# Kernel tuning notes

Measured on AMD Instinct MI355X. Metric: run time of the kernel, lower is better.

Reference implementation:

```python
import jax, jax.numpy as jnp
import numpy as np

SLOPE = 0.2  # leaky_relu_slope for both LVC block and kernel predictor (passed through)
DILATIONS = (1, 3, 9, 27)
HOP = 256
STRIDE = 8
IN_CH = 32
KSZ = 3  # conv_kernel_size


def conv1d(x, w, b, dilation=1, padding=0):
    # x: (B,C,T), w: (O,I,K) torch layout
    y = jax.lax.conv_general_dilated(
        x, w, window_strides=(1,), padding=[(padding, padding)],
        rhs_dilation=(dilation,), dimension_numbers=('NCH', 'OIH', 'NCH'))
    return y + b[None, :, None]


def conv_transpose1d(x, w, b, stride, padding, output_padding=0):
    # w: torch ConvTranspose1d layout (Cin, Cout, K)
    w_ = jnp.flip(w, -1).transpose(1, 0, 2)  # (Cout, Cin, K)
    K = w.shape[2]
    pad = (K - 1 - padding, K - 1 - padding + output_padding)
    y = jax.lax.conv_general_dilated(
        x, w_, window_strides=(1,), padding=[pad],
        lhs_dilation=(stride,), dimension_numbers=('NCH', 'OIH', 'NCH'))
    return y + b[None, :, None]


def lrelu(x, slope=SLOPE):
    return jnp.where(x >= 0, x, slope * x)


def location_variable_convolution(x, kernel, bias, hop):
    # x: (B,C,T), kernel: (B,C,O,k,L), bias: (B,O,L); T == L*hop; dilation==1 path
    B, C, T = x.shape
    _, _, O, k, L = kernel.shape
    pad = (k - 1) // 2
    xp = jnp.pad(x, ((0, 0), (0, 0), (pad, pad)))
    # gather per-segment sliding windows: (L, hop, k) index into time axis
    idx = (jnp.arange(L)[:, None, None] * hop
           + jnp.arange(hop)[None, :, None]
           + jnp.arange(k)[None, None, :])
    xw = xp[:, :, idx]  # (B, C, L, hop, k)
    o = jnp.einsum('bclsk,bcokl->bols', xw, kernel)  # (B, O, L, hop)
    o = o + bias[:, :, :, None]
    return o.reshape(B, O, L * hop)


def kernel_predictor(spec, kp_in_w, kp_in_b, rb_w1, rb_b1, rb_w2, rb_b2,
                     kern_w, kern_b, bias_w, bias_b):
    B, _, L = spec.shape
    h = conv1d(spec, kp_in_w, kp_in_b, padding=2)  # k=5, pad=2
    for i in range(3):  # num_blocks = 3
        r = h
        h = conv1d(h, rb_w1[i], rb_b1[i], padding=1)
        h = lrelu(h)
        h = conv1d(h, rb_w2[i], rb_b2[i], padding=1)
        h = lrelu(h) + r
    kh = conv1d(h, kern_w, kern_b, padding=1)
    bh = conv1d(h, bias_w, bias_b, padding=1)
    n_layers = len(DILATIONS)
    kernels = kh.reshape(B, n_layers, IN_CH, 2 * IN_CH, KSZ, L)
    biases = bh.reshape(B, n_layers, 2 * IN_CH, L)
    return kernels, biases


def reference(hidden_states, spectrogram, convt_w, convt_b, kp_in_w, kp_in_b,
              rb_w1, rb_b1, rb_w2, rb_b2, kern_w, kern_b, bias_w, bias_b,
              lvc_w, lvc_b):
    h = conv_transpose1d(hidden_states, convt_w, convt_b,
                         stride=STRIDE, padding=STRIDE // 2 + STRIDE % 2,
                         output_padding=STRIDE % 2)
    kernels, biases = kernel_predictor(spectrogram, kp_in_w, kp_in_b,
                                       rb_w1, rb_b1, rb_w2, rb_b2,
                                       kern_w, kern_b, bias_w, bias_b)
    for i, d in enumerate(DILATIONS):
        r = h
        h = lrelu(h)
        h = conv1d(h, lvc_w[i], lvc_b[i], dilation=d, padding=d * (KSZ - 1) // 2)
        h = lrelu(h)
        h = location_variable_convolution(h, kernels[:, i], biases[:, i], HOP)
        h = jax.nn.sigmoid(h[:, :IN_CH, :]) * jnp.tanh(h[:, IN_CH:, :]) + r
    return h


def setup_inputs() -> dict:
    key = jax.random.key(0)
    ks = jax.random.split(key, 12)
    B, COND, L, H = 4, 100, 256, 64
    T = L * HOP  # 65536 output samples
    s = jnp.float32(0.02)
    d = {}
    d['hidden_states'] = jax.random.normal(ks[0], (B, IN_CH, T // STRIDE), jnp.float32)
    d['spectrogram'] = jax.random.normal(ks[1], (B, COND, L), jnp.float32)
    d['convt_w'] = jax.random.normal(ks[2], (IN_CH, IN_CH, 2 * STRIDE), jnp.float32) * s
    d['convt_b'] = jnp.zeros((IN_CH,), jnp.float32)
    d['kp_in_w'] = jax.random.normal(ks[3], (H, COND, 5), jnp.float32) * s
    d['kp_in_b'] = jnp.zeros((H,), jnp.float32)
    d['rb_w1'] = jax.random.normal(ks[4], (3, H, H, 3), jnp.float32) * s
    d['rb_b1'] = jnp.zeros((3, H), jnp.float32)
    d['rb_w2'] = jax.random.normal(ks[5], (3, H, H, 3), jnp.float32) * s
    d['rb_b2'] = jnp.zeros((3, H), jnp.float32)
    KC = IN_CH * 2 * IN_CH * KSZ * len(DILATIONS)  # 24576
    d['kern_w'] = jax.random.normal(ks[6], (KC, H, 3), jnp.float32) * s
    d['kern_b'] = jnp.zeros((KC,), jnp.float32)
    BC = 2 * IN_CH * len(DILATIONS)  # 256
    d['bias_w'] = jax.random.normal(ks[7], (BC, H, 3), jnp.float32) * s
    d['bias_b'] = jnp.zeros((BC,), jnp.float32)
    d['lvc_w'] = jax.random.normal(ks[8], (len(DILATIONS), IN_CH, IN_CH, 3), jnp.float32) * s
    d['lvc_b'] = jnp.zeros((len(DILATIONS), IN_CH), jnp.float32)
    return d
```

## Files before the change

### kernel.cpp

```cpp
#include <hip/hip_runtime.h>
#include <math.h>

#define NB 4
#define T 65536
#define TIN 8192
#define LL 256
#define KCL 6144

__device__ __forceinline__ float lrelu_f(float v) { return v >= 0.f ? v : 0.2f * v; }

union Phase1LDS {
    struct { float xs[32][264]; float wm[64][128]; } cvt;
    struct { float hs[64][56]; float xsp[20][56]; float wt[192][68]; } trk;
};

__global__ void __launch_bounds__(512) phase1(
    const float* __restrict__ x, const float* __restrict__ cw,
    const float* __restrict__ cbias, float* __restrict__ hout,
    const float* __restrict__ spec,
    const float* __restrict__ kp_in_w, const float* __restrict__ kp_in_b,
    const float* __restrict__ rb_w1, const float* __restrict__ rb_b1,
    const float* __restrict__ rb_w2, const float* __restrict__ rb_b2,
    float* __restrict__ kp_h) {
    __shared__ Phase1LDS u;
    const int bid = blockIdx.x;
    const int tid = threadIdx.x;
    const int lane = tid & 63, wv = tid >> 6;

    if (bid < 264) {
        const int bx = bid % 33;
        const int rr = bid / 33;
        const int mtp = rr & 1;
        const int b = rr >> 1;
        const int s0base = bx * 256;
        float (*xs)[264] = u.cvt.xs;
        float (*wm)[128] = u.cvt.wm;

        const float* xb = x + (size_t)b * 32 * TIN;
        for (int idx = tid; idx < 32 * 64; idx += 512) {
            int c = idx >> 6, q = idx & 63;
            int p = s0base + q * 4;
            float4 v = (p + 3 < TIN) ? *(const float4*)(xb + c * TIN + p)
                                     : make_float4(0.f, 0.f, 0.f, 0.f);
            *(float4*)&xs[c][4 + 4 * q] = v;
        }
        if (tid < 32) {
            int p = s0base - 1;
            xs[tid][3] = (p >= 0) ? xb[tid * TIN + p] : 0.f;
        }
        for (int idx = tid; idx < 8192; idx += 512) {
            int i = idx >> 7, mm = idx & 127;
            int oo = mtp * 16 + (mm >> 3), k0 = mm & 7;
            wm[i][mm] = (i < 32) ? cw[i * 512 + oo * 16 + k0]
                                 : cw[(i - 32) * 512 + oo * 16 + k0 + 8];
        }
        __syncthreads();

        float acc[2][8][4];
#pragma unroll
        for (int ol = 0; ol < 2; ++ol) {
            float bo = cbias[mtp * 16 + wv * 2 + ol];
#pragma unroll
            for (int k0 = 0; k0 < 8; ++k0)
#pragma unroll
                for (int si = 0; si < 4; ++si) acc[ol][k0][si] = bo;
        }

        for (int c = 0; c < 32; ++c) {
            float xm1[4], x0[4];
#pragma unroll
            for (int si = 0; si < 4; ++si) {
                xm1[si] = xs[c][lane + si * 64 + 3];
                x0[si]  = xs[c][lane + si * 64 + 4];
            }
            float w0[16], w1[16];
#pragma unroll
            for (int q = 0; q < 4; ++q) {
                *(float4*)&w0[q * 4] = *(const float4*)&wm[c][wv * 16 + q * 4];
                *(float4*)&w1[q * 4] = *(const float4*)&wm[32 + c][wv * 16 + q * 4];
            }
#pragma unroll
            for (int ol = 0; ol < 2; ++ol)
#pragma unroll
                for (int k0 = 0; k0 < 8; ++k0)
#pragma unroll
                    for (int si = 0; si < 4; ++si)
                        acc[ol][k0][si] += x0[si] * w0[ol * 8 + k0] + xm1[si] * w1[ol * 8 + k0];
        }

#pragma unroll
        for (int ol = 0; ol < 2; ++ol) {
            float* ob = hout + ((size_t)b * 32 + mtp * 16 + wv * 2 + ol) * T;
#pragma unroll
            for (int si = 0; si < 4; ++si) {
                int tb = (s0base + lane + si * 64) * 8 - 4;
                if (tb >= 0 && tb < T)
                    *(float4*)(ob + tb) = make_float4(acc[ol][0][si], acc[ol][1][si],
                                                      acc[ol][2][si], acc[ol][3][si]);
                if (tb + 4 >= 0 && tb + 4 < T)
                    *(float4*)(ob + tb + 4) = make_float4(acc[ol][4][si], acc[ol][5][si],
                                                          acc[ol][6][si], acc[ol][7][si]);
            }
        }
        return;
    }

    const int tb = bid - 264;
    const int lq = tb & 7, b = tb >> 3;
    const int j = lane;
    const int oc0 = wv * 8;
    const int l0 = lq * 32;
    const int labs = l0 - 9 + j;
    const bool lvalid = (labs >= 0 && labs < 256);

    float (*hs)[56] = u.trk.hs;
    float (*xsp)[56] = u.trk.xsp;
    float (*wt)[68] = u.trk.wt;

    float pw[24];
    float px[3];

    auto pf_kpin = [&](int cc) {
#pragma unroll
        for (int t = 0; t < 13; ++t) {
            int idx = t * 512 + tid;
            pw[t] = 0.f;
            if (idx < 6400) pw[t] = kp_in_w[(size_t)(idx / 100) * 500 + cc * 100 + (idx % 100)];
        }
    };
    auto wr_kpin = [&]() {
#pragma unroll
        for (int t = 0; t < 13; ++t) {
            int idx = t * 512 + tid;
            if (idx < 6400) wt[idx % 100][idx / 100] = pw[t];
        }
    };
    auto pf_xsp = [&](int cc) {
#pragma unroll
        for (int t = 0; t < 3; ++t) {
            int idx = t * 512 + tid;
            px[t] = 0.f;
            if (idx < 1120) {
                int c = idx / 56, jj = idx - c * 56;
                int l = l0 - 9 + jj;
                if (l >= 0 && l < 256)
                    px[t] = spec[((size_t)b * 100 + cc * 20 + c) * LL + l];
            }
        }
    };
    auto wr_xsp = [&]() {
#pragma unroll
        for (int t = 0; t < 3; ++t) {
            int idx = t * 512 + tid;
            if (idx < 1120) xsp[idx / 56][idx % 56] = px[t];
        }
    };
    auto pf_w192 = [&](const float* src) {
#pragma unroll
        for (int t = 0; t < 24; ++t) pw[t] = src[t * 512 + tid];
    };
    auto wr_w192 = [&]() {
#pragma unroll
        for (int t = 0; t < 24; ++t) {
            int idx = t * 512 + tid;
            wt[idx % 192][idx / 192] = pw[t];
        }
    };
    auto conv64 = [&](int jlo, int jhi, const float* bptr, float* a) {
#pragma unroll
        for (int oi = 0; oi < 8; ++oi) a[oi] = bptr[oc0 + oi];
        if (j >= jlo && j < jhi) {
            for (int c = 0; c < 64; ++c) {
                float x0 = hs[c][j - 1], x1 = hs[c][j], x2 = hs[c][j + 1];
#pragma unroll
                for (int k = 0; k < 3; ++k) {
                    float xk = (k == 0) ? x0 : (k == 1) ? x1 : x2;
                    float w8[8];
                    *(float4*)&w8[0] = *(const float4*)&wt[c * 3 + k][oc0];
                    *(float4*)&w8[4] = *(const float4*)&wt[c * 3 + k][oc0 + 4];
#pragma unroll
                    for (int oi = 0; oi < 8; ++oi) a[oi] += xk * w8[oi];
                }
            }
        }
    };

    pf_kpin(0); pf_xsp(0);
    wr_kpin(); wr_xsp();
    __syncthreads();

    float acc[8];
#pragma unroll
    for (int oi = 0; oi < 8; ++oi) acc[oi] = kp_in_b[oc0 + oi];

    for (int cc = 0; cc < 5; ++cc) {
        if (cc < 4) { pf_kpin(cc + 1); pf_xsp(cc + 1); }
        else        { pf_w192(rb_w1); }
        if (j >= 2 && j < 48) {
            for (int c = 0; c < 20; ++c) {
                float x5[5];
#pragma unroll
                for (int u2 = 0; u2 < 5; ++u2) x5[u2] = xsp[c][j - 2 + u2];
#pragma unroll
                for (int k = 0; k < 5; ++k) {
                    float w8[8];
                    *(float4*)&w8[0] = *(const float4*)&wt[c * 5 + k][oc0];
                    *(float4*)&w8[4] = *(const float4*)&wt[c * 5 + k][oc0 + 4];
#pragma unroll
                    for (int oi = 0; oi < 8; ++oi) acc[oi] += x5[k] * w8[oi];
                }
            }
        }
        if (cc == 4 && j >= 2 && j < 48) {
#pragma unroll
            for (int oi = 0; oi < 8; ++oi) hs[oc0 + oi][j] = lvalid ? acc[oi] : 0.f;
        }
        __syncthreads();
        if (cc < 4) { wr_kpin(); wr_xsp(); }
        else        { wr_w192(); }
        __syncthreads();
    }

    for (int i = 0; i < 3; ++i) {
        const int jlo1 = 3 + 2 * i, jhi1 = 47 - 2 * i;
        const int jlo2 = jlo1 + 1, jhi2 = jhi1 - 1;
        float r[8];
        if (j >= jlo2 && j < jhi2) {
#pragma unroll
            for (int oi = 0; oi < 8; ++oi) r[oi] = hs[oc0 + oi][j];
        }
        pf_w192(rb_w2 + (size_t)i * 12288);
        float a1[8];
        conv64(jlo1, jhi1, rb_b1 + i * 64, a1);
        __syncthreads();
        if (j >= jlo1 && j < jhi1) {
#pragma unroll
            for (int oi = 0; oi < 8; ++oi) hs[oc0 + oi][j] = lvalid ? lrelu_f(a1[oi]) : 0.f;
        }
        wr_w192();
        __syncthreads();
        if (i < 2) pf_w192(rb_w1 + (size_t)(i + 1) * 12288);
        float a2[8];
        conv64(jlo2, jhi2, rb_b2 + i * 64, a2);
        __syncthreads();
        if (j >= jlo2 && j < jhi2) {
#pragma unroll
            for (int oi = 0; oi < 8; ++oi) hs[oc0 + oi][j] = lvalid ? (lrelu_f(a2[oi]) + r[oi]) : 0.f;
        }
        if (i < 2) wr_w192();
        __syncthreads();
    }

    for (int idx = tid; idx < 64 * 32; idx += 512) {
        int c = idx >> 5, jj = idx & 31;
        kp_h[((size_t)b * 64 + c) * LL + l0 + jj] = hs[c][9 + jj];
    }
}

__device__ __forceinline__ void khead_core(
    int bx, int b, int tid,
    const float* __restrict__ kp_h, const float* __restrict__ kw,
    const float* __restrict__ kb, const float* __restrict__ bias_w,
    const float* __restrict__ bias_b, float* __restrict__ kh,
    float* __restrict__ bh, int layer,
    float (*xs)[264], float (*ws)[36]) {
    const bool isbias = (bx >= 192);
    const int lane = tid & 63, wv = tid >> 6;
    int g = 0, oc0 = 0, ci = 0, kk = 0, ocb0 = 0;
    const float* wsrc;
    size_t wrow0;
    int wstride;
    if (!isbias) {
        g = bx >> 1; oc0 = (bx & 1) * 32;
        ci = g / 3; kk = g - ci * 3;
        wsrc = kw + (size_t)layer * KCL * 192;
        wrow0 = (size_t)((ci * 64 + oc0) * 3 + kk) * 192;
        wstride = 576;
    } else {
        ocb0 = (bx - 192) * 32;
        wsrc = bias_w;
        wrow0 = (size_t)ocb0 * 192;
        wstride = 192;
    }
    const int oc4w = wv * 4;

    float acc[4][4];
#pragma unroll
    for (int oi = 0; oi < 4; ++oi) {
        float bv = isbias ? bias_b[ocb0 + oc4w + oi]
                          : kb[layer * KCL + (ci * 64 + oc0 + oc4w + oi) * 3 + kk];
#pragma unroll
        for (int q = 0; q < 4; ++q) acc[oi][q] = bv;
    }

    for (int half = 0; half < 2; ++half) {
        const int hc0 = half * 32;
        __syncthreads();
        for (int idx = tid; idx < 32 * 64; idx += 512) {
            int c = idx >> 6, q = idx & 63;
            *(float4*)&xs[c][4 + 4 * q] =
                *(const float4*)(kp_h + ((size_t)b * 64 + hc0 + c) * LL + 4 * q);
        }
        if (tid < 32) { xs[tid][3] = 0.f; xs[tid][260] = 0.f; }
        for (int idx = tid; idx < 3072; idx += 512) {
            int ocl = idx / 96, jj = idx - ocl * 96;
            ws[jj][ocl] = wsrc[wrow0 + (size_t)ocl * wstride + hc0 * 3 + jj];
        }
        __syncthreads();
        for (int c = 0; c < 32; ++c) {
            float4 xa = *(const float4*)&xs[c][4 * lane];
            float4 xm = *(const float4*)&xs[c][4 + 4 * lane];
            float4 xb = *(const float4*)&xs[c][8 + 4 * lane];
            float xx[6] = {xa.w, xm.x, xm.y, xm.z, xm.w, xb.x};
#pragma unroll
            for (int t = 0; t < 3; ++t) {
                float4 w4 = *(const float4*)&ws[c * 3 + t][oc4w];
#pragma unroll
                for (int q = 0; q < 4; ++q) {
                    acc[0][q] += w4.x * xx[q + t];
                    acc[1][q] += w4.y * xx[q + t];
                    acc[2][q] += w4.z * xx[q + t];
                    acc[3][q] += w4.w * xx[q + t];
                }
            }
        }
    }

    if (!isbias) {
#pragma unroll
        for (int q = 0; q < 4; ++q) {
            int l = 4 * lane + q;
            float* op = kh + ((size_t)b * LL + l) * KCL + g * 64 + oc0 + oc4w;
            *(float4*)op = make_float4(acc[0][q], acc[1][q], acc[2][q], acc[3][q]);
        }
    } else {
#pragma unroll
        for (int oi = 0; oi < 4; ++oi) {
            float* op = bh + ((size_t)b * 256 + ocb0 + oc4w + oi) * LL + 4 * lane;
            *(float4*)op = make_float4(acc[oi][0], acc[oi][1], acc[oi][2], acc[oi][3]);
        }
    }
}

__global__ void __launch_bounds__(512, 2) kern_head512(
    const float* __restrict__ kp_h, const float* __restrict__ kw,
    const float* __restrict__ kb, const float* __restrict__ bias_w,
    const float* __restrict__ bias_b, float* __restrict__ kh,
    float* __restrict__ bh, int layer) {
    __shared__ float xs[32][264];
    __shared__ float ws[96][36];
    khead_core(blockIdx.x, blockIdx.y, threadIdx.x, kp_h, kw, kb, bias_w, bias_b,
               kh, bh, layer, xs, ws);
}

__device__ __forceinline__ void lf_core(
    int l, int b, int tid,
    const float* __restrict__ kh, const float* __restrict__ bh,
    const float* __restrict__ w, const float* __restrict__ bias,
    const float* __restrict__ hin, float* __restrict__ hout,
    int layer, int dil,
    float (*xh)[316], float* ks, float (*ws)[36]) {
    const int lane = tid & 63, wv = tid >> 6;
    const int t0 = l * 256;

    const float* hb = hin + (size_t)b * 32 * T;
    for (int idx = tid; idx < 32 * 64; idx += 512) {
        int c = idx >> 6, q = idx & 63;
        float4 v = *(const float4*)(hb + (size_t)c * T + t0 + 4 * q);
        *(float4*)&xh[c][32 + 4 * q] = make_float4(lrelu_f(v.x), lrelu_f(v.y),
                                                   lrelu_f(v.z), lrelu_f(v.w));
    }
    for (int idx = tid; idx < 32 * 60; idx += 512) {
        int c = idx / 60, r = idx - c * 60;
        int jj = (r < 32) ? r : (256 + r);
        int t = t0 + jj - 32;
        xh[c][jj] = (t >= 0 && t < T) ? lrelu_f(hb[(size_t)c * T + t]) : 0.f;
    }
    {
        const float4* kp = (const float4*)(kh + ((size_t)b * LL + l) * KCL);
        float4* kd = (float4*)ks;
        for (int idx = tid; idx < KCL / 4; idx += 512) kd[idx] = kp[idx];
    }
    for (int idx = tid; idx < 3072; idx += 512) {
        int oc = idx / 96, ck = idx - oc * 96;
        ws[ck][oc] = w[oc * 96 + ck];
    }
    __syncthreads();

    const int oc4 = wv * 4;
    float yv[5][4];
    {
        float a[5][4];
#pragma unroll
        for (int oi = 0; oi < 4; ++oi) {
            float bv = bias[oc4 + oi];
#pragma unroll
            for (int si = 0; si < 5; ++si) a[si][oi] = bv;
        }
        for (int c = 0; c < 32; ++c) {
#pragma unroll
            for (int k = 0; k < 3; ++k) {
                float4 wq = *(const float4*)&ws[c * 3 + k][oc4];
                float xv[5];
#pragma unroll
                for (int si = 0; si < 5; ++si) {
                    int col = lane + si * 64;
                    int colc = (col < 258) ? col : 257;
                    xv[si] = xh[c][colc + 31 + (k - 1) * dil];
                }
#pragma unroll
                for (int si = 0; si < 5; ++si) {
                    a[si][0] += xv[si] * wq.x;
                    a[si][1] += xv[si] * wq.y;
                    a[si][2] += xv[si] * wq.z;
                    a[si][3] += xv[si] * wq.w;
                }
            }
        }
#pragma unroll
        for (int si = 0; si < 5; ++si) {
            int t = t0 - 1 + lane + si * 64;
            bool tval = (t >= 0 && t < T);
#pragma unroll
            for (int oi = 0; oi < 4; ++oi)
                yv[si][oi] = tval ? lrelu_f(a[si][oi]) : 0.f;
        }
    }
    __syncthreads();

#pragma unroll
    for (int si = 0; si < 5; ++si) {
        int col = lane + si * 64;
        if (col < 258) {
#pragma unroll
            for (int oi = 0; oi < 4; ++oi) xh[oc4 + oi][col + 31] = yv[si][oi];
        }
    }
    __syncthreads();

    float acc_a[4][4], acc_g[4][4];
#pragma unroll
    for (int oi = 0; oi < 4; ++oi) {
        float ba = bh[((size_t)b * 256 + layer * 64 + oc4 + oi) * LL + l];
        float bg = bh[((size_t)b * 256 + layer * 64 + 32 + oc4 + oi) * LL + l];
#pragma unroll
        for (int si = 0; si < 4; ++si) { acc_a[oi][si] = ba; acc_g[oi][si] = bg; }
    }

    for (int c = 0; c < 32; ++c) {
#pragma unroll
        for (int k = 0; k < 3; ++k) {
            const float* kr = ks + (c * 3 + k) * 64;
            float4 wa = *(const float4*)(kr + oc4);
            float4 wg = *(const float4*)(kr + 32 + oc4);
            float xv[4];
#pragma unroll
            for (int si = 0; si < 4; ++si)
                xv[si] = xh[c][lane + si * 64 + k + 31];
#pragma unroll
            for (int si = 0; si < 4; ++si) {
                acc_a[0][si] += wa.x * xv[si];
                acc_a[1][si] += wa.y * xv[si];
                acc_a[2][si] += wa.z * xv[si];
                acc_a[3][si] += wa.w * xv[si];
                acc_g[0][si] += wg.x * xv[si];
                acc_g[1][si] += wg.y * xv[si];
                acc_g[2][si] += wg.z * xv[si];
                acc_g[3][si] += wg.w * xv[si];
            }
        }
    }

#pragma unroll
    for (int oi = 0; oi < 4; ++oi) {
        const float* hip = hin + ((size_t)b * 32 + oc4 + oi) * T + t0;
        float* hop = hout + ((size_t)b * 32 + oc4 + oi) * T + t0;
#pragma unroll
        for (int si = 0; si < 4; ++si) {
            int s = lane + si * 64;
            float a = acc_a[oi][si], g = acc_g[oi][si];
            float sg = 1.f / (1.f + __expf(-a));
            float th = tanhf(g);
            hop[s] = sg * th + hip[s];
        }
    }
}

union FusedLDS {
    struct { float xh[32][316]; float ks[KCL]; float ws[96][36]; } lf;
    struct { float xs[32][264]; float ws[96][36]; } kh;
};

__global__ void __launch_bounds__(512, 2) fused(
    const float* __restrict__ kp_h, const float* __restrict__ kw,
    const float* __restrict__ kb, const float* __restrict__ bias_w,
    const float* __restrict__ bias_b,
    const float* __restrict__ kh_rd, float* __restrict__ kh_wr,
    float* __restrict__ bh,
    const float* __restrict__ lvcw, const float* __restrict__ lvcb,
    const float* __restrict__ hin, float* __restrict__ hout,
    int lf_layer, int dil, int kh_on) {
    __shared__ FusedLDS u;
    const int g = blockIdx.x;
    const int tid = threadIdx.x;
    if (kh_on) {
        const int r = g % 7, q7 = g / 7;
        if (r < 3) {
            const int ukh = q7 * 3 + r;
            const int bx = ukh % 192, b = ukh / 192;
            khead_core(bx, b, tid, kp_h, kw, kb, bias_w, bias_b,
                       kh_wr, bh, lf_layer + 1, u.kh.xs, u.kh.ws);
            return;
        }
        const int ulf = q7 * 4 + (r - 3);
        lf_core(ulf & 255, ulf >> 8, tid, kh_rd, bh, lvcw, lvcb,
                hin, hout, lf_layer, dil, u.lf.xh, u.lf.ks, u.lf.ws);
    } else {
        lf_core(g & 255, g >> 8, tid, kh_rd, bh, lvcw, lvcb,
                hin, hout, lf_layer, dil, u.lf.xh, u.lf.ks, u.lf.ws);
    }
}

extern "C" void kernel_launch(void* const* d_in, const int* in_sizes, int n_in,
                              void* d_out, int out_size, void* d_ws, size_t ws_size,
                              hipStream_t stream) {
    const float* hidden  = (const float*)d_in[0];
    const float* spec    = (const float*)d_in[1];
    const float* convt_w = (const float*)d_in[2];
    const float* convt_b = (const float*)d_in[3];
    const float* kp_in_w = (const float*)d_in[4];
    const float* kp_in_b = (const float*)d_in[5];
    const float* rb_w1   = (const float*)d_in[6];
    const float* rb_b1   = (const float*)d_in[7];
    const float* rb_w2   = (const float*)d_in[8];
    const float* rb_b2   = (const float*)d_in[9];
    const float* kern_w  = (const float*)d_in[10];
    const float* kern_b  = (const float*)d_in[11];
    const float* bias_w  = (const float*)d_in[12];
    const float* bias_b  = (const float*)d_in[13];
    const float* lvc_w   = (const float*)d_in[14];
    const float* lvc_b   = (const float*)d_in[15];

    const size_t NH  = (size_t)NB * 32 * T;
    const size_t NKH = (size_t)NB * LL * KCL;
    const size_t NBH = (size_t)NB * 256 * LL;
    const size_t NKP = (size_t)NB * 64 * LL;
    const size_t need_pp = (NH + 2 * NKH + NBH + NKP) * sizeof(float);
    const bool pp = ws_size >= need_pp;

    float* wsp  = (float*)d_ws;
    float* h_ws = wsp;
    float* kh0  = h_ws + NH;
    float* kh1  = pp ? (kh0 + NKH) : kh0;
    float* bh   = (pp ? kh1 : kh0) + NKH;
    float* kp_h = bh + NBH;

    float* h0 = (float*)d_out;
    float* h1 = h_ws;

    phase1<<<dim3(296), 512, 0, stream>>>(hidden, convt_w, convt_b, h0,
                                          spec, kp_in_w, kp_in_b,
                                          rb_w1, rb_b1, rb_w2, rb_b2, kp_h);

    kern_head512<<<dim3(200, NB), 512, 0, stream>>>(
        kp_h, kern_w, kern_b, bias_w, bias_b, kh0, bh, 0);

    static const int dil[4] = {1, 3, 9, 27};
    float* hin = h0;
    float* hout = h1;
    for (int l = 0; l < 4; ++l) {
        const float* rd = (l & 1) ? kh1 : kh0;
        float* wr = (l & 1) ? kh0 : kh1;
        if (pp && l < 3) {
            fused<<<dim3(1792), 512, 0, stream>>>(
                kp_h, kern_w, kern_b, bias_w, bias_b, rd, wr, bh,
                lvc_w + (size_t)l * 32 * 32 * 3, lvc_b + l * 32,
                hin, hout, l, dil[l], 1);
        } else {
            fused<<<dim3(1024), 512, 0, stream>>>(
                kp_h, kern_w, kern_b, bias_w, bias_b, rd, (float*)rd, bh,
                lvc_w + (size_t)l * 32 * 32 * 3, lvc_b + l * 32,
                hin, hout, l, dil[l], 0);
            if (!pp && l < 3)
                kern_head512<<<dim3(192, NB), 512, 0, stream>>>(
                    kp_h, kern_w, kern_b, bias_w, bias_b, kh0, bh, l + 1);
        }
        float* tmp = hin; hin = hout; hout = tmp;
    }
}
```

Baseline: 751.8 us.

## Widen kernel-head tiles to 64 output channels per block and rebalance fused grid

Each kernel-head block now computes all 64 output channels of a (ci,k) group instead of 32, with each thread holding an 8x4 register tile. This halves the number of kernel-head blocks and reloads of the shared input slab. The interleaving in the fused kernel changes from 3:4 to 3:8 kernel-head to LVC blocks to match the smaller head block count. The cost is more registers per thread and a larger weight tile in LDS. Thread-to-time mapping also switches from contiguous groups of 4 to a stride of 64, which changes how LDS reads and global stores are coalesced.

```diff
diff --git a/kernel.cpp b/kernel.cpp
--- a/kernel.cpp
+++ b/kernel.cpp
@@ -263,34 +263,37 @@
     const float* __restrict__ kb, const float* __restrict__ bias_w,
     const float* __restrict__ bias_b, float* __restrict__ kh,
     float* __restrict__ bh, int layer,
-    float (*xs)[264], float (*ws)[36]) {
-    const bool isbias = (bx >= 192);
+    float (*xs)[264], float (*ws)[68]) {
+    const bool isbias = (bx >= 96);
     const int lane = tid & 63, wv = tid >> 6;
-    int g = 0, oc0 = 0, ci = 0, kk = 0, ocb0 = 0;
+    int g = 0, ci = 0, kk = 0, ocb0 = 0;
     const float* wsrc;
     size_t wrow0;
-    int wstride;
+    int wstride, nst;
     if (!isbias) {
-        g = bx >> 1; oc0 = (bx & 1) * 32;
-        ci = g / 3; kk = g - ci * 3;
+        g = bx; ci = g / 3; kk = g - ci * 3;
         wsrc = kw + (size_t)layer * KCL * 192;
-        wrow0 = (size_t)((ci * 64 + oc0) * 3 + kk) * 192;
+        wrow0 = (size_t)(ci * 192 + kk) * 192;
         wstride = 576;
+        nst = 96 * 64;
     } else {
-        ocb0 = (bx - 192) * 32;
+        ocb0 = (bx - 96) * 32;
         wsrc = bias_w;
         wrow0 = (size_t)ocb0 * 192;
         wstride = 192;
-    }
+        nst = 96 * 32;
+    }
+    const int oc8 = wv * 8;
     const int oc4w = wv * 4;
 
-    float acc[4][4];
-#pragma unroll
-    for (int oi = 0; oi < 4; ++oi) {
-        float bv = isbias ? bias_b[ocb0 + oc4w + oi]
-                          : kb[layer * KCL + (ci * 64 + oc0 + oc4w + oi) * 3 + kk];
-#pragma unroll
-        for (int q = 0; q < 4; ++q) acc[oi][q] = bv;
+    float acc[8][4];
+#pragma unroll
+    for (int oi = 0; oi < 8; ++oi) {
+        float bv;
+        if (isbias) bv = (oi < 4) ? bias_b[ocb0 + oc4w + oi] : 0.f;
+        else        bv = kb[layer * KCL + (ci * 64 + oc8 + oi) * 3 + kk];
+#pragma unroll
+        for (int si = 0; si < 4; ++si) acc[oi][si] = bv;
     }
 
     for (int half = 0; half < 2; ++half) {
@@ -302,42 +305,63 @@
                 *(const float4*)(kp_h + ((size_t)b * 64 + hc0 + c) * LL + 4 * q);
         }
         if (tid < 32) { xs[tid][3] = 0.f; xs[tid][260] = 0.f; }
-        for (int idx = tid; idx < 3072; idx += 512) {
+        for (int idx = tid; idx < nst; idx += 512) {
             int ocl = idx / 96, jj = idx - ocl * 96;
             ws[jj][ocl] = wsrc[wrow0 + (size_t)ocl * wstride + hc0 * 3 + jj];
         }
         __syncthreads();
-        for (int c = 0; c < 32; ++c) {
-            float4 xa = *(const float4*)&xs[c][4 * lane];
-            float4 xm = *(const float4*)&xs[c][4 + 4 * lane];
-            float4 xb = *(const float4*)&xs[c][8 + 4 * lane];
-            float xx[6] = {xa.w, xm.x, xm.y, xm.z, xm.w, xb.x};
-#pragma unroll
-            for (int t = 0; t < 3; ++t) {
-                float4 w4 = *(const float4*)&ws[c * 3 + t][oc4w];
-#pragma unroll
-                for (int q = 0; q < 4; ++q) {
-                    acc[0][q] += w4.x * xx[q + t];
-                    acc[1][q] += w4.y * xx[q + t];
-                    acc[2][q] += w4.z * xx[q + t];
-                    acc[3][q] += w4.w * xx[q + t];
+        if (!isbias) {
+            for (int c = 0; c < 32; ++c) {
+#pragma unroll
+                for (int t = 0; t < 3; ++t) {
+                    float w8[8];
+                    *(float4*)&w8[0] = *(const float4*)&ws[c * 3 + t][oc8];
+                    *(float4*)&w8[4] = *(const float4*)&ws[c * 3 + t][oc8 + 4];
+                    float xv[4];
+#pragma unroll
+                    for (int si = 0; si < 4; ++si) xv[si] = xs[c][lane + si * 64 + t + 3];
+#pragma unroll
+                    for (int oi = 0; oi < 8; ++oi)
+#pragma unroll
+                        for (int si = 0; si < 4; ++si)
+                            acc[oi][si] += w8[oi] * xv[si];
                 }
             }
+        } else {
+            for (int c = 0; c < 32; ++c) {
+#pragma unroll
+                for (int t = 0; t < 3; ++t) {
+                    float4 w4 = *(const float4*)&ws[c * 3 + t][oc4w];
+                    float xv[4];
+#pragma unroll
+                    for (int si = 0; si < 4; ++si) xv[si] = xs[c][lane + si * 64 + t + 3];
+#pragma unroll
+                    for (int si = 0; si < 4; ++si) {
+                        acc[0][si] += w4.x * xv[si];
+                        acc[1][si] += w4.y * xv[si];
+                        acc[2][si] += w4.z * xv[si];
+                        acc[3][si] += w4.w * xv[si];
+                    }
+                }
+            }
         }
     }
 
     if (!isbias) {
 #pragma unroll
-        for (int q = 0; q < 4; ++q) {
-            int l = 4 * lane + q;
-            float* op = kh + ((size_t)b * LL + l) * KCL + g * 64 + oc0 + oc4w;
-            *(float4*)op = make_float4(acc[0][q], acc[1][q], acc[2][q], acc[3][q]);
+        for (int si = 0; si < 4; ++si) {
+            int l = lane + si * 64;
+            float* op = kh + ((size_t)b * LL + l) * KCL + g * 64 + oc8;
+            *(float4*)(op)     = make_float4(acc[0][si], acc[1][si], acc[2][si], acc[3][si]);
+            *(float4*)(op + 4) = make_float4(acc[4][si], acc[5][si], acc[6][si], acc[7][si]);
         }
     } else {
 #pragma unroll
         for (int oi = 0; oi < 4; ++oi) {
-            float* op = bh + ((size_t)b * 256 + ocb0 + oc4w + oi) * LL + 4 * lane;
-            *(float4*)op = make_float4(acc[oi][0], acc[oi][1], acc[oi][2], acc[oi][3]);
+            float* op = bh + ((size_t)b * 256 + ocb0 + oc4w + oi) * LL;
+#pragma unroll
+            for (int si = 0; si < 4; ++si)
+                op[lane + si * 64] = acc[oi][si];
         }
     }
 }
@@ -348,7 +372,7 @@
     const float* __restrict__ bias_b, float* __restrict__ kh,
     float* __restrict__ bh, int layer) {
     __shared__ float xs[32][264];
-    __shared__ float ws[96][36];
+    __shared__ float ws[96][68];
     khead_core(blockIdx.x, blockIdx.y, threadIdx.x, kp_h, kw, kb, bias_w, bias_b,
                kh, bh, layer, xs, ws);
 }
@@ -488,7 +512,7 @@
 
 union FusedLDS {
     struct { float xh[32][316]; float ks[KCL]; float ws[96][36]; } lf;
-    struct { float xs[32][264]; float ws[96][36]; } kh;
+    struct { float xs[32][264]; float ws[96][68]; } kh;
 };
 
 __global__ void __launch_bounds__(512, 2) fused(
@@ -504,15 +528,15 @@
     const int g = blockIdx.x;
     const int tid = threadIdx.x;
     if (kh_on) {
-        const int r = g % 7, q7 = g / 7;
+        const int r = g % 11, q11 = g / 11;
         if (r < 3) {
-            const int ukh = q7 * 3 + r;
-            const int bx = ukh % 192, b = ukh / 192;
+            const int ukh = q11 * 3 + r;
+            const int bx = ukh % 96, b = ukh / 96;
             khead_core(bx, b, tid, kp_h, kw, kb, bias_w, bias_b,
                        kh_wr, bh, lf_layer + 1, u.kh.xs, u.kh.ws);
             return;
         }
-        const int ulf = q7 * 4 + (r - 3);
+        const int ulf = q11 * 8 + (r - 3);
         lf_core(ulf & 255, ulf >> 8, tid, kh_rd, bh, lvcw, lvcb,
                 hin, hout, lf_layer, dil, u.lf.xh, u.lf.ks, u.lf.ws);
     } else {
@@ -562,7 +586,7 @@
                                           spec, kp_in_w, kp_in_b,
                                           rb_w1, rb_b1, rb_w2, rb_b2, kp_h);
 
-    kern_head512<<<dim3(200, NB), 512, 0, stream>>>(
+    kern_head512<<<dim3(104, NB), 512, 0, stream>>>(
         kp_h, kern_w, kern_b, bias_w, bias_b, kh0, bh, 0);
 
     static const int dil[4] = {1, 3, 9, 27};
@@ -572,7 +596,7 @@
         const float* rd = (l & 1) ? kh1 : kh0;
         float* wr = (l & 1) ? kh0 : kh1;
         if (pp && l < 3) {
-            fused<<<dim3(1792), 512, 0, stream>>>(
+            fused<<<dim3(1408), 512, 0, stream>>>(
                 kp_h, kern_w, kern_b, bias_w, bias_b, rd, wr, bh,
                 lvc_w + (size_t)l * 32 * 32 * 3, lvc_b + l * 32,
                 hin, hout, l, dil[l], 1);
@@ -582,7 +606,7 @@
                 lvc_w + (size_t)l * 32 * 32 * 3, lvc_b + l * 32,
                 hin, hout, l, dil[l], 0);
             if (!pp && l < 3)
-                kern_head512<<<dim3(192, NB), 512, 0, stream>>>(
+                kern_head512<<<dim3(96, NB), 512, 0, stream>>>(
                     kp_h, kern_w, kern_b, bias_w, bias_b, kh0, bh, l + 1);
         }
         float* tmp = hin; hin = hout; hout = tmp;
```

After: 667.5 us. 1.13x faster.
